# Optimization experiments

Hardware: AMD Instinct MI355X
Metric: run time of the kernel (lower is better)

## Reference

```python
import jax, jax.numpy as jnp
import numpy as np

B, T, C = 2, 2048, 2048
N_HEADS, HEAD_DIM, N_KV_HEADS = 16, 128, 4
N_REP = N_HEADS // N_KV_HEADS
WINDOW = 512
EPS = 1e-6
THETA = 10000.0


def setup_inputs() -> dict:
    key = jax.random.key(0)
    ks = jax.random.split(key, 6)
    x = jax.random.normal(ks[0], (B, T, C), dtype=jnp.float32)
    norm_w = jnp.ones((C,), dtype=jnp.float32)
    wq = jax.random.normal(ks[1], (C, N_HEADS * HEAD_DIM), dtype=jnp.float32) * 0.02
    wk = jax.random.normal(ks[2], (C, N_KV_HEADS * HEAD_DIM), dtype=jnp.float32) * 0.02
    wv = jax.random.normal(ks[3], (C, N_KV_HEADS * HEAD_DIM), dtype=jnp.float32) * 0.02
    wo = jax.random.normal(ks[4], (N_HEADS * HEAD_DIM, C), dtype=jnp.float32) * 0.02
    # precompute_rope: freqs over half head_dim, outer with positions
    inv = 1.0 / (THETA ** (np.arange(0, HEAD_DIM, 2, dtype=np.float32) / HEAD_DIM))
    t = np.arange(T, dtype=np.float32)
    freqs = np.outer(t, inv)  # (T, HEAD_DIM/2)
    rope_cos = jnp.asarray(np.cos(freqs), dtype=jnp.float32)
    rope_sin = jnp.asarray(np.sin(freqs), dtype=jnp.float32)
    return {"x": x, "norm_w": norm_w, "wq": wq, "wk": wk, "wv": wv, "wo": wo,
            "rope_cos": rope_cos, "rope_sin": rope_sin}


def _rmsnorm(x, w):
    xf = x.astype(jnp.float32)
    norm = jax.lax.rsqrt(jnp.mean(xf * xf, axis=-1, keepdims=True) + EPS)
    return (xf * norm).astype(x.dtype) * w


def _rotate(x, cos, sin):
    # x: (B,H,T,D); cos/sin: (1,1,T,D/2). Half-split RoPE as in apply_rope.
    d = x.shape[-1] // 2
    x1, x2 = x[..., :d], x[..., d:]
    return jnp.concatenate([x1 * cos - x2 * sin, x2 * cos + x1 * sin], axis=-1)


def reference(x, norm_w, wq, wk, wv, wo, rope_cos, rope_sin):
    normed = _rmsnorm(x, norm_w)
    q = (normed @ wq).reshape(B, T, N_HEADS, HEAD_DIM).transpose(0, 2, 1, 3)
    k = (normed @ wk).reshape(B, T, N_KV_HEADS, HEAD_DIM).transpose(0, 2, 1, 3)
    v = (normed @ wv).reshape(B, T, N_KV_HEADS, HEAD_DIM).transpose(0, 2, 1, 3)
    cos = rope_cos[None, None, :T, :]
    sin = rope_sin[None, None, :T, :]
    q = _rotate(q, cos, sin)
    k = _rotate(k, cos, sin)
    # GQA: repeat each kv head contiguously (matches expand+reshape)
    k = jnp.repeat(k, N_REP, axis=1)
    v = jnp.repeat(v, N_REP, axis=1)
    scale = 1.0 / jnp.sqrt(jnp.float32(HEAD_DIM))
    scores = jnp.einsum('bhtd,bhsd->bhts', q, k) * scale  # (B,H,T,T)
    # causal + sliding window mask (S == T, offset == 0)
    row = jnp.arange(T)[:, None]
    col = jnp.arange(T)[None, :]
    mask = (col <= row) & (row - col < WINDOW)  # (T,T) bool
    scores = jnp.where(mask[None, None, :, :], scores, -jnp.inf)
    attn = jax.nn.softmax(scores, axis=-1)
    out = jnp.einsum('bhts,bhsd->bhtd', attn, v)
    out = out.transpose(0, 2, 1, 3).reshape(B, T, N_HEADS * HEAD_DIM)
    return x + out @ wo
```

## Files before the change

kernel.cpp:

```cpp
#include <hip/hip_runtime.h>
#include <hip/hip_bf16.h>

typedef __attribute__((ext_vector_type(8))) __bf16 bf16x8;
typedef __attribute__((ext_vector_type(4))) __bf16 bf16x4;
typedef __attribute__((ext_vector_type(4))) float f32x4;

#define BDIM 2
#define TSEQ 2048
#define CDIM 2048
#define NH 16
#define NKV 4
#define HD 128
#define WIN 512

__device__ __forceinline__ void gl_lds16(const __bf16* g, __bf16* l) {
  __builtin_amdgcn_global_load_lds(
      (const __attribute__((address_space(1))) void*)g,
      (__attribute__((address_space(3))) void*)l, 16, 0, 0);
}

__global__ __launch_bounds__(256) void k_rmsnorm(const float* __restrict__ x,
                                                 const float* __restrict__ w,
                                                 __bf16* __restrict__ xn) {
  __shared__ float red[4];
  const int row = blockIdx.x;
  const int tid = threadIdx.x;
  const float* xr = x + (size_t)row * CDIM;
  f32x4 v0 = *reinterpret_cast<const f32x4*>(&xr[tid * 8]);
  f32x4 v1 = *reinterpret_cast<const f32x4*>(&xr[tid * 8 + 4]);
  float s = v0[0] * v0[0] + v0[1] * v0[1] + v0[2] * v0[2] + v0[3] * v0[3] +
            v1[0] * v1[0] + v1[1] * v1[1] + v1[2] * v1[2] + v1[3] * v1[3];
#pragma unroll
  for (int off = 32; off > 0; off >>= 1) s += __shfl_down(s, off, 64);
  if ((tid & 63) == 0) red[tid >> 6] = s;
  __syncthreads();
  float tot = red[0] + red[1] + red[2] + red[3];
  float nrm = rsqrtf(tot * (1.0f / CDIM) + 1e-6f);
  const float* wp = w + tid * 8;
  bf16x8 o;
  o[0] = (__bf16)(v0[0] * nrm * wp[0]);
  o[1] = (__bf16)(v0[1] * nrm * wp[1]);
  o[2] = (__bf16)(v0[2] * nrm * wp[2]);
  o[3] = (__bf16)(v0[3] * nrm * wp[3]);
  o[4] = (__bf16)(v1[0] * nrm * wp[4]);
  o[5] = (__bf16)(v1[1] * nrm * wp[5]);
  o[6] = (__bf16)(v1[2] * nrm * wp[6]);
  o[7] = (__bf16)(v1[3] * nrm * wp[7]);
  *reinterpret_cast<bf16x8*>(&xn[(size_t)row * CDIM + tid * 8]) = o;
}

__global__ __launch_bounds__(256) void k_wtrans_all(
    const float* __restrict__ wq, const float* __restrict__ wk,
    const float* __restrict__ wv, const float* __restrict__ wo,
    __bf16* __restrict__ wqT, __bf16* __restrict__ wkT,
    __bf16* __restrict__ wvT, __bf16* __restrict__ woT) {
  __shared__ float lt[64][65];
  const int bx = blockIdx.x;
  const float* W;
  __bf16* Wt;
  int N, ntile;
  if (bx < 32) { W = wq; Wt = wqT; N = 2048; ntile = bx; }
  else if (bx < 40) { W = wk; Wt = wkT; N = 512; ntile = bx - 32; }
  else if (bx < 48) { W = wv; Wt = wvT; N = 512; ntile = bx - 40; }
  else { W = wo; Wt = woT; N = 2048; ntile = bx - 48; }
  const int tid = threadIdx.x;
  const int n0 = ntile * 64, k0 = blockIdx.y * 64;
  const int tr = tid >> 4, tc = tid & 15;
#pragma unroll
  for (int i = 0; i < 4; ++i) {
    int kr = tr + i * 16;
    f32x4 vv = *reinterpret_cast<const f32x4*>(&W[(size_t)(k0 + kr) * N + n0 + tc * 4]);
    lt[kr][tc * 4 + 0] = vv[0];
    lt[kr][tc * 4 + 1] = vv[1];
    lt[kr][tc * 4 + 2] = vv[2];
    lt[kr][tc * 4 + 3] = vv[3];
  }
  __syncthreads();
#pragma unroll
  for (int i = 0; i < 4; ++i) {
    int nr = tr + i * 16;
    int kc = tc * 4;
    bf16x4 o;
    o[0] = (__bf16)lt[kc + 0][nr];
    o[1] = (__bf16)lt[kc + 1][nr];
    o[2] = (__bf16)lt[kc + 2][nr];
    o[3] = (__bf16)lt[kc + 3][nr];
    *reinterpret_cast<bf16x4*>(&Wt[(size_t)(n0 + nr) * 2048 + k0 + kc]) = o;
  }
}

__global__ __launch_bounds__(256) void k_rope(__bf16* __restrict__ Q,
                                              __bf16* __restrict__ K,
                                              const float* __restrict__ rc,
                                              const float* __restrict__ rs) {
  int g = blockIdx.x * 4 + (threadIdx.x >> 6);
  int lane = threadIdx.x & 63;
  int b = g / (TSEQ * (NH + NKV));
  int rem = g % (TSEQ * (NH + NKV));
  int t = rem / (NH + NKV);
  int hh = rem % (NH + NKV);
  __bf16* base;
  if (hh < NH)
    base = Q + (((size_t)(b * NH + hh)) * TSEQ + t) * HD;
  else
    base = K + (((size_t)(b * NKV + (hh - NH))) * TSEQ + t) * HD;
  float x1 = (float)base[lane];
  float x2 = (float)base[lane + 64];
  float c = rc[t * 64 + lane];
  float s = rs[t * 64 + lane];
  base[lane] = (__bf16)(x1 * c - x2 * s);
  base[lane + 64] = (__bf16)(x2 * c + x1 * s);
}

__global__ __launch_bounds__(256) void k_gemm_qkv(
    const __bf16* __restrict__ xn, const __bf16* __restrict__ wqT,
    const __bf16* __restrict__ wkT, const __bf16* __restrict__ wvT,
    __bf16* __restrict__ Q, __bf16* __restrict__ K, __bf16* __restrict__ VT) {
  __shared__ __align__(16) __bf16 lmem[128 * 136];
  __bf16* lA = lmem;
  __bf16* lB = lmem + 128 * 32;
  const int tid = threadIdx.x;
  const int lane = tid & 63;
  const int w = tid >> 6;
  const int wrow = (w >> 1) * 64, wcol = (w & 1) * 64;
  const int l16 = lane & 15, lhi = lane >> 4;
  const int grow = lane >> 2;
  const int gcol = (lane & 3) * 8;
  const int m0 = blockIdx.y * 128;
  const int n0 = blockIdx.x * 128;
  const __bf16* wt;
  int nrel;
  if (n0 < 2048) { wt = wqT; nrel = n0; }
  else if (n0 < 2560) { wt = wkT; nrel = n0 - 2048; }
  else { wt = wvT; nrel = n0 - 2560; }

  f32x4 acc[4][4] = {};

  for (int k0 = 0; k0 < CDIM; k0 += 32) {
#pragma unroll
    for (int i = 0; i < 2; ++i) {
      const int r0 = (w * 2 + i) * 16;
      gl_lds16(&xn[(size_t)(m0 + r0 + grow) * CDIM + k0 + gcol], &lA[r0 * 32]);
      gl_lds16(&wt[(size_t)(nrel + r0 + grow) * CDIM + k0 + gcol], &lB[r0 * 32]);
    }
    __syncthreads();
    bf16x8 a[4], b[4];
#pragma unroll
    for (int mi = 0; mi < 4; ++mi)
      a[mi] = *reinterpret_cast<const bf16x8*>(&lA[(wrow + mi * 16 + l16) * 32 + lhi * 8]);
#pragma unroll
    for (int ni = 0; ni < 4; ++ni)
      b[ni] = *reinterpret_cast<const bf16x8*>(&lB[(wcol + ni * 16 + l16) * 32 + lhi * 8]);
#pragma unroll
    for (int mi = 0; mi < 4; ++mi)
#pragma unroll
      for (int ni = 0; ni < 4; ++ni)
        acc[mi][ni] = __builtin_amdgcn_mfma_f32_16x16x32_bf16(a[mi], b[ni], acc[mi][ni], 0, 0, 0);
    __syncthreads();
  }

  const int bb = m0 >> 11;
  if (n0 < 2560) {
#pragma unroll
    for (int mi = 0; mi < 4; ++mi) {
#pragma unroll
      for (int ni = 0; ni < 4; ++ni) {
#pragma unroll
        for (int r = 0; r < 4; ++r) {
          int row = m0 + wrow + mi * 16 + lhi * 4 + r;
          int col = n0 + wcol + ni * 16 + l16;
          int t = row & 2047;
          __bf16 hv = (__bf16)acc[mi][ni][r];
          if (n0 < 2048) {
            int h = col >> 7, d = col & 127;
            Q[(((size_t)(bb * NH + h)) * TSEQ + t) * HD + d] = hv;
          } else {
            int h = (col - 2048) >> 7, d = col & 127;
            K[(((size_t)(bb * NKV + h)) * TSEQ + t) * HD + d] = hv;
          }
        }
      }
    }
  } else {
#pragma unroll
    for (int mi = 0; mi < 4; ++mi)
#pragma unroll
      for (int ni = 0; ni < 4; ++ni)
#pragma unroll
        for (int r = 0; r < 4; ++r)
          lmem[(size_t)(wcol + ni * 16 + l16) * 136 + wrow + mi * 16 + lhi * 4 + r] =
              (__bf16)acc[mi][ni][r];
    __syncthreads();
    const int h = (n0 - 2560) >> 7;
    const size_t vbase = ((size_t)(bb * NKV + h)) * HD * TSEQ;
    const int t0 = m0 & 2047;
#pragma unroll
    for (int it = 0; it < 8; ++it) {
      int d = it * 16 + (tid >> 4);
      int tt = (tid & 15) * 8;
      bf16x8 vv = *reinterpret_cast<const bf16x8*>(&lmem[(size_t)d * 136 + tt]);
      *reinterpret_cast<bf16x8*>(&VT[vbase + (size_t)d * TSEQ + t0 + tt]) = vv;
    }
  }
}

#define SWZ(row, col) ((col) ^ (((row) & 7) << 3))

__global__ __launch_bounds__(256) void k_attn(const __bf16* __restrict__ Q,
                                              const __bf16* __restrict__ K,
                                              const __bf16* __restrict__ VT,
                                              __bf16* __restrict__ Aout) {
  __shared__ __align__(16) __bf16 lK[64 * 128];
  __shared__ __align__(16) __bf16 lVt[128 * 64];
  __shared__ __align__(16) __bf16 lP[4][32][68];

  const int tid = threadIdx.x, lane = tid & 63, wid = tid >> 6;
  const int l16 = lane & 15, lhi = lane >> 4;
  const int bh = blockIdx.y;
  const int b = bh >> 4, h = bh & 15;
  const int kvh = h >> 2;
  const int qb = 15 - blockIdx.x;
  const int q0 = qb * 128;
  const int qw = q0 + wid * 32;

  const __bf16* Qb = Q + (size_t)bh * TSEQ * HD;
  const __bf16* Kb = K + (size_t)(b * NKV + kvh) * TSEQ * HD;
  const __bf16* Vt = VT + (size_t)(b * NKV + kvh) * HD * TSEQ;

  bf16x8 aq[2][4];
#pragma unroll
  for (int mi = 0; mi < 2; ++mi)
#pragma unroll
    for (int dblk = 0; dblk < 4; ++dblk)
      aq[mi][dblk] = *reinterpret_cast<const bf16x8*>(
          &Qb[(size_t)(qw + mi * 16 + l16) * HD + dblk * 32 + lhi * 8]);

  float mrow[2][4], lrow[2][4];
#pragma unroll
  for (int mi = 0; mi < 2; ++mi)
#pragma unroll
    for (int r = 0; r < 4; ++r) { mrow[mi][r] = -INFINITY; lrow[mi][r] = 0.0f; }
  f32x4 accO[2][8] = {};

  int s_lo = q0 - (WIN - 1);
  if (s_lo < 0) s_lo = 0;
  s_lo &= ~63;
  const int nt = (q0 + 128 - s_lo) >> 6;
  const float scale = 0.08838834764831845f;

  const int krow = tid >> 4, kcol = (tid & 15) * 8;
  bf16x8 kreg[4], vreg[4];
#pragma unroll
  for (int i = 0; i < 4; ++i) {
    int slot = tid + i * 256;
    kreg[i] = *reinterpret_cast<const bf16x8*>(
        &Kb[(size_t)(s_lo + (slot >> 4)) * HD + (slot & 15) * 8]);
    vreg[i] = *reinterpret_cast<const bf16x8*>(
        &Vt[(size_t)(slot >> 3) * TSEQ + s_lo + (slot & 7) * 8]);
  }

  for (int t = 0; t < nt; ++t) {
    const int s0 = s_lo + t * 64;
    __syncthreads();
#pragma unroll
    for (int i = 0; i < 4; ++i) {
      int slot = tid + i * 256;
      int kr = slot >> 4, kc = (slot & 15) * 8;
      *reinterpret_cast<bf16x8*>(&lK[kr * 128 + SWZ(kr, kc)]) = kreg[i];
      int vd = slot >> 3, vc = (slot & 7) * 8;
      *reinterpret_cast<bf16x8*>(&lVt[vd * 64 + SWZ(vd, vc)]) = vreg[i];
    }
    if (t + 1 < nt) {
      const int s1 = s0 + 64;
#pragma unroll
      for (int i = 0; i < 4; ++i) {
        int slot = tid + i * 256;
        kreg[i] = *reinterpret_cast<const bf16x8*>(
            &Kb[(size_t)(s1 + (slot >> 4)) * HD + (slot & 15) * 8]);
        vreg[i] = *reinterpret_cast<const bf16x8*>(
            &Vt[(size_t)(slot >> 3) * TSEQ + s1 + (slot & 7) * 8]);
      }
    }
    __syncthreads();

#pragma unroll
    for (int mi = 0; mi < 2; ++mi) {
      f32x4 accS[4] = {};
      __builtin_amdgcn_s_setprio(1);
#pragma unroll
      for (int sb = 0; sb < 4; ++sb) {
#pragma unroll
        for (int dblk = 0; dblk < 4; ++dblk) {
          int srow = sb * 16 + l16, scol = dblk * 32 + lhi * 8;
          bf16x8 bk = *reinterpret_cast<const bf16x8*>(&lK[srow * 128 + SWZ(srow, scol)]);
          accS[sb] = __builtin_amdgcn_mfma_f32_16x16x32_bf16(aq[mi][dblk], bk, accS[sb], 0, 0, 0);
        }
      }
      __builtin_amdgcn_s_setprio(0);
#pragma unroll
      for (int r = 0; r < 4; ++r) {
        int qrow = qw + mi * 16 + lhi * 4 + r;
        float vv[4];
        float tmax = -INFINITY;
#pragma unroll
        for (int sb = 0; sb < 4; ++sb) {
          int sc = s0 + sb * 16 + l16;
          float val = accS[sb][r] * scale;
          bool ok = (sc <= qrow) && (qrow - sc < WIN);
          vv[sb] = ok ? val : -INFINITY;
          tmax = fmaxf(tmax, vv[sb]);
        }
#pragma unroll
        for (int off = 1; off < 16; off <<= 1) tmax = fmaxf(tmax, __shfl_xor(tmax, off, 64));
        float mnew = fmaxf(mrow[mi][r], tmax);
        float msafe = (mnew == -INFINITY) ? 0.0f : mnew;
        float corr = (mrow[mi][r] == mnew) ? 1.0f : __expf(mrow[mi][r] - mnew);
        float psum = 0.0f;
#pragma unroll
        for (int sb = 0; sb < 4; ++sb) {
          float p = __expf(vv[sb] - msafe);
          psum += p;
          lP[wid][mi * 16 + lhi * 4 + r][sb * 16 + l16] = (__bf16)p;
        }
#pragma unroll
        for (int off = 1; off < 16; off <<= 1) psum += __shfl_xor(psum, off, 64);
        lrow[mi][r] = lrow[mi][r] * corr + psum;
        mrow[mi][r] = mnew;
#pragma unroll
        for (int ni = 0; ni < 8; ++ni) accO[mi][ni][r] *= corr;
      }
    }

    bf16x8 ap[2][2];
#pragma unroll
    for (int mi = 0; mi < 2; ++mi)
#pragma unroll
      for (int ks = 0; ks < 2; ++ks)
        ap[mi][ks] = *reinterpret_cast<const bf16x8*>(&lP[wid][mi * 16 + l16][ks * 32 + lhi * 8]);
    __builtin_amdgcn_s_setprio(1);
#pragma unroll
    for (int ni = 0; ni < 8; ++ni) {
      int vrow = ni * 16 + l16;
      bf16x8 bv0 = *reinterpret_cast<const bf16x8*>(&lVt[vrow * 64 + SWZ(vrow, lhi * 8)]);
      bf16x8 bv1 = *reinterpret_cast<const bf16x8*>(&lVt[vrow * 64 + SWZ(vrow, 32 + lhi * 8)]);
      accO[0][ni] = __builtin_amdgcn_mfma_f32_16x16x32_bf16(ap[0][0], bv0, accO[0][ni], 0, 0, 0);
      accO[0][ni] = __builtin_amdgcn_mfma_f32_16x16x32_bf16(ap[0][1], bv1, accO[0][ni], 0, 0, 0);
      accO[1][ni] = __builtin_amdgcn_mfma_f32_16x16x32_bf16(ap[1][0], bv0, accO[1][ni], 0, 0, 0);
      accO[1][ni] = __builtin_amdgcn_mfma_f32_16x16x32_bf16(ap[1][1], bv1, accO[1][ni], 0, 0, 0);
    }
    __builtin_amdgcn_s_setprio(0);
  }

#pragma unroll
  for (int mi = 0; mi < 2; ++mi) {
    float invl[4];
#pragma unroll
    for (int r = 0; r < 4; ++r) invl[r] = 1.0f / lrow[mi][r];
#pragma unroll
    for (int ni = 0; ni < 8; ++ni) {
#pragma unroll
      for (int r = 0; r < 4; ++r) {
        int row = qw + mi * 16 + lhi * 4 + r;
        int d = ni * 16 + l16;
        Aout[((size_t)(b * TSEQ + row)) * CDIM + h * HD + d] = (__bf16)(accO[mi][ni][r] * invl[r]);
      }
    }
  }
}

__global__ __launch_bounds__(256) void k_gemm_out(const __bf16* __restrict__ A,
                                                  const __bf16* __restrict__ woT,
                                                  const float* __restrict__ x,
                                                  float* __restrict__ out) {
  __shared__ __align__(16) __bf16 lA[128 * 32];
  __shared__ __align__(16) __bf16 lB[128 * 32];
  const int tid = threadIdx.x;
  const int lane = tid & 63;
  const int w = tid >> 6;
  const int wrow = (w >> 1) * 64, wcol = (w & 1) * 64;
  const int l16 = lane & 15, lhi = lane >> 4;
  const int grow = lane >> 2;
  const int gcol = (lane & 3) * 8;
  const int m0 = blockIdx.y * 128;
  const int n0 = blockIdx.x * 128;

  f32x4 acc[4][4] = {};

  for (int k0 = 0; k0 < CDIM; k0 += 32) {
#pragma unroll
    for (int i = 0; i < 2; ++i) {
      const int r0 = (w * 2 + i) * 16;
      gl_lds16(&A[(size_t)(m0 + r0 + grow) * CDIM + k0 + gcol], &lA[r0 * 32]);
      gl_lds16(&woT[(size_t)(n0 + r0 + grow) * CDIM + k0 + gcol], &lB[r0 * 32]);
    }
    __syncthreads();
    bf16x8 a[4], b[4];
#pragma unroll
    for (int mi = 0; mi < 4; ++mi)
      a[mi] = *reinterpret_cast<const bf16x8*>(&lA[(wrow + mi * 16 + l16) * 32 + lhi * 8]);
#pragma unroll
    for (int ni = 0; ni < 4; ++ni)
      b[ni] = *reinterpret_cast<const bf16x8*>(&lB[(wcol + ni * 16 + l16) * 32 + lhi * 8]);
#pragma unroll
    for (int mi = 0; mi < 4; ++mi)
#pragma unroll
      for (int ni = 0; ni < 4; ++ni)
        acc[mi][ni] = __builtin_amdgcn_mfma_f32_16x16x32_bf16(a[mi], b[ni], acc[mi][ni], 0, 0, 0);
    __syncthreads();
  }

#pragma unroll
  for (int mi = 0; mi < 4; ++mi) {
#pragma unroll
    for (int ni = 0; ni < 4; ++ni) {
#pragma unroll
      for (int r = 0; r < 4; ++r) {
        int row = m0 + wrow + mi * 16 + lhi * 4 + r;
        int col = n0 + wcol + ni * 16 + l16;
        size_t idx = (size_t)row * CDIM + col;
        out[idx] = x[idx] + acc[mi][ni][r];
      }
    }
  }
}

extern "C" void kernel_launch(void* const* d_in, const int* in_sizes, int n_in,
                              void* d_out, int out_size, void* d_ws, size_t ws_size,
                              hipStream_t stream) {
  const float* x = (const float*)d_in[0];
  const float* norm_w = (const float*)d_in[1];
  const float* wq = (const float*)d_in[2];
  const float* wk = (const float*)d_in[3];
  const float* wv = (const float*)d_in[4];
  const float* wo = (const float*)d_in[5];
  const float* rc = (const float*)d_in[6];
  const float* rs = (const float*)d_in[7];
  float* out = (float*)d_out;

  char* ws = (char*)d_ws;
  __bf16* xn  = (__bf16*)(ws);
  __bf16* wqT = (__bf16*)(ws + 16777216);
  __bf16* wkT = (__bf16*)(ws + 25165824);
  __bf16* wvT = (__bf16*)(ws + 27262976);
  __bf16* woT = (__bf16*)(ws + 29360128);
  __bf16* Qb  = (__bf16*)(ws + 37748736);
  __bf16* Kb  = (__bf16*)(ws + 54525952);
  __bf16* VTb = (__bf16*)(ws + 58720256);
  if (ws_size < 62914560) return;

  k_wtrans_all<<<dim3(80, 32), 256, 0, stream>>>(wq, wk, wv, wo, wqT, wkT, wvT, woT);
  k_rmsnorm<<<4096, 256, 0, stream>>>(x, norm_w, xn);
  k_gemm_qkv<<<dim3(24, 32), 256, 0, stream>>>(xn, wqT, wkT, wvT, Qb, Kb, VTb);
  k_rope<<<(BDIM * TSEQ * (NH + NKV)) / 4, 256, 0, stream>>>(Qb, Kb, rc, rs);
  k_attn<<<dim3(16, BDIM * NH), 256, 0, stream>>>(Qb, Kb, VTb, xn);
  k_gemm_out<<<dim3(16, 32), 256, 0, stream>>>(xn, woT, x, out);
}
```

Measured before the change: 330.8 us.

## Compute transposed S tile so softmax rows live per lane, add lazy rescaling

Swaps the MFMA operands so each lane holds one query row across 16 key columns, cutting the per-row shuffle reductions from four steps per row to two cross-group shuffles. It adds a FlashAttention-4 style deferred max update: rescaling of the O accumulator is skipped when no row's max grows by more than 8. P is written to LDS as packed bf16x4 with a padded stride of 72. The trade-off is extra __shfl calls to broadcast correction factors back to the accumulator layout, and probabilities up to e^8 stored in bf16.

New measurement: 304.8 us. 7.8% less time.

```diff
diff --git a/kernel.cpp b/kernel.cpp
--- a/kernel.cpp
+++ b/kernel.cpp
@@ -205,6 +205,7 @@
 }
 
 #define SWZ(row, col) ((col) ^ (((row) & 7) << 3))
+#define LPS 72
 
 __global__ __launch_bounds__(256) void k_attn(const __bf16* __restrict__ Q,
                                               const __bf16* __restrict__ K,
@@ -212,7 +213,7 @@
                                               __bf16* __restrict__ Aout) {
   __shared__ __align__(16) __bf16 lK[64 * 128];
   __shared__ __align__(16) __bf16 lVt[128 * 64];
-  __shared__ __align__(16) __bf16 lP[4][32][68];
+  __shared__ __align__(16) __bf16 lP[4][32][LPS];
 
   const int tid = threadIdx.x, lane = tid & 63, wid = tid >> 6;
   const int l16 = lane & 15, lhi = lane >> 4;
@@ -235,11 +236,8 @@
       aq[mi][dblk] = *reinterpret_cast<const bf16x8*>(
           &Qb[(size_t)(qw + mi * 16 + l16) * HD + dblk * 32 + lhi * 8]);
 
-  float mrow[2][4], lrow[2][4];
-#pragma unroll
-  for (int mi = 0; mi < 2; ++mi)
-#pragma unroll
-    for (int r = 0; r < 4; ++r) { mrow[mi][r] = -INFINITY; lrow[mi][r] = 0.0f; }
+  float mrow[2] = {-INFINITY, -INFINITY};
+  float lrow[2] = {0.0f, 0.0f};
   f32x4 accO[2][8] = {};
 
   int s_lo = q0 - (WIN - 1);
@@ -248,7 +246,6 @@
   const int nt = (q0 + 128 - s_lo) >> 6;
   const float scale = 0.08838834764831845f;
 
-  const int krow = tid >> 4, kcol = (tid & 15) * 8;
   bf16x8 kreg[4], vreg[4];
 #pragma unroll
   for (int i = 0; i < 4; ++i) {
@@ -283,52 +280,71 @@
     }
     __syncthreads();
 
+    f32x4 accT[2][4] = {};
+    __builtin_amdgcn_s_setprio(1);
+#pragma unroll
+    for (int sb = 0; sb < 4; ++sb) {
+#pragma unroll
+      for (int dblk = 0; dblk < 4; ++dblk) {
+        int srow = sb * 16 + l16, scol = dblk * 32 + lhi * 8;
+        bf16x8 bk = *reinterpret_cast<const bf16x8*>(&lK[srow * 128 + SWZ(srow, scol)]);
+        accT[0][sb] = __builtin_amdgcn_mfma_f32_16x16x32_bf16(bk, aq[0][dblk], accT[0][sb], 0, 0, 0);
+        accT[1][sb] = __builtin_amdgcn_mfma_f32_16x16x32_bf16(bk, aq[1][dblk], accT[1][sb], 0, 0, 0);
+      }
+    }
+    __builtin_amdgcn_s_setprio(0);
+
 #pragma unroll
     for (int mi = 0; mi < 2; ++mi) {
-      f32x4 accS[4] = {};
-      __builtin_amdgcn_s_setprio(1);
+      const int qrow = qw + mi * 16 + l16;
+      float pv[4][4];
+      float tmax = -INFINITY;
 #pragma unroll
       for (int sb = 0; sb < 4; ++sb) {
 #pragma unroll
-        for (int dblk = 0; dblk < 4; ++dblk) {
-          int srow = sb * 16 + l16, scol = dblk * 32 + lhi * 8;
-          bf16x8 bk = *reinterpret_cast<const bf16x8*>(&lK[srow * 128 + SWZ(srow, scol)]);
-          accS[sb] = __builtin_amdgcn_mfma_f32_16x16x32_bf16(aq[mi][dblk], bk, accS[sb], 0, 0, 0);
+        for (int r = 0; r < 4; ++r) {
+          int sc = s0 + sb * 16 + lhi * 4 + r;
+          float val = accT[mi][sb][r] * scale;
+          bool ok = (sc <= qrow) && (qrow - sc < WIN);
+          val = ok ? val : -INFINITY;
+          pv[sb][r] = val;
+          tmax = fmaxf(tmax, val);
         }
       }
-      __builtin_amdgcn_s_setprio(0);
-#pragma unroll
-      for (int r = 0; r < 4; ++r) {
-        int qrow = qw + mi * 16 + lhi * 4 + r;
-        float vv[4];
-        float tmax = -INFINITY;
-#pragma unroll
-        for (int sb = 0; sb < 4; ++sb) {
-          int sc = s0 + sb * 16 + l16;
-          float val = accS[sb][r] * scale;
-          bool ok = (sc <= qrow) && (qrow - sc < WIN);
-          vv[sb] = ok ? val : -INFINITY;
-          tmax = fmaxf(tmax, vv[sb]);
+      tmax = fmaxf(tmax, __shfl_xor(tmax, 16, 64));
+      tmax = fmaxf(tmax, __shfl_xor(tmax, 32, 64));
+
+      bool defer = __all(tmax <= mrow[mi] + 8.0f);
+      float mnew = mrow[mi];
+      if (!defer) {
+        mnew = fmaxf(mrow[mi], tmax);
+        float corr = (mrow[mi] == mnew) ? 1.0f : __expf(mrow[mi] - mnew);
+        mrow[mi] = mnew;
+        lrow[mi] *= corr;
+        float corrR[4];
+#pragma unroll
+        for (int r = 0; r < 4; ++r) corrR[r] = __shfl(corr, lhi * 4 + r, 64);
+#pragma unroll
+        for (int ni = 0; ni < 8; ++ni)
+#pragma unroll
+          for (int r = 0; r < 4; ++r) accO[mi][ni][r] *= corrR[r];
+      }
+      float msafe = (mnew == -INFINITY) ? 0.0f : mnew;
+      float psum = 0.0f;
+#pragma unroll
+      for (int sb = 0; sb < 4; ++sb) {
+        bf16x4 pk;
+#pragma unroll
+        for (int r = 0; r < 4; ++r) {
+          float p = __expf(pv[sb][r] - msafe);
+          psum += p;
+          pk[r] = (__bf16)p;
         }
-#pragma unroll
-        for (int off = 1; off < 16; off <<= 1) tmax = fmaxf(tmax, __shfl_xor(tmax, off, 64));
-        float mnew = fmaxf(mrow[mi][r], tmax);
-        float msafe = (mnew == -INFINITY) ? 0.0f : mnew;
-        float corr = (mrow[mi][r] == mnew) ? 1.0f : __expf(mrow[mi][r] - mnew);
-        float psum = 0.0f;
-#pragma unroll
-        for (int sb = 0; sb < 4; ++sb) {
-          float p = __expf(vv[sb] - msafe);
-          psum += p;
-          lP[wid][mi * 16 + lhi * 4 + r][sb * 16 + l16] = (__bf16)p;
-        }
-#pragma unroll
-        for (int off = 1; off < 16; off <<= 1) psum += __shfl_xor(psum, off, 64);
-        lrow[mi][r] = lrow[mi][r] * corr + psum;
-        mrow[mi][r] = mnew;
-#pragma unroll
-        for (int ni = 0; ni < 8; ++ni) accO[mi][ni][r] *= corr;
-      }
+        *reinterpret_cast<bf16x4*>(&lP[wid][mi * 16 + l16][sb * 16 + lhi * 4]) = pk;
+      }
+      psum += __shfl_xor(psum, 16, 64);
+      psum += __shfl_xor(psum, 32, 64);
+      lrow[mi] += psum;
     }
 
     bf16x8 ap[2][2];
@@ -353,16 +369,17 @@
 
 #pragma unroll
   for (int mi = 0; mi < 2; ++mi) {
-    float invl[4];
-#pragma unroll
-    for (int r = 0; r < 4; ++r) invl[r] = 1.0f / lrow[mi][r];
+    float invl = 1.0f / lrow[mi];
+    float invlR[4];
+#pragma unroll
+    for (int r = 0; r < 4; ++r) invlR[r] = __shfl(invl, lhi * 4 + r, 64);
 #pragma unroll
     for (int ni = 0; ni < 8; ++ni) {
 #pragma unroll
       for (int r = 0; r < 4; ++r) {
         int row = qw + mi * 16 + lhi * 4 + r;
         int d = ni * 16 + l16;
-        Aout[((size_t)(b * TSEQ + row)) * CDIM + h * HD + d] = (__bf16)(accO[mi][ni][r] * invl[r]);
+        Aout[((size_t)(b * TSEQ + row)) * CDIM + h * HD + d] = (__bf16)(accO[mi][ni][r] * invlR[r]);
       }
     }
   }
```
